# Optimization experiments

Hardware: AMD Instinct MI355X
Metric: run time of the kernel (lower is better)

The kernel has to match this reference:

```python
import jax, jax.numpy as jnp
import numpy as np

D_MODEL = 256
D_HEAD = 64
N_HEAD = 8


def setup_inputs() -> dict:
    key = jax.random.key(0)
    ks = jax.random.split(key, 8)
    b, h, w = 32, 64, 64
    dk = D_HEAD * N_HEAD
    s = 1.0 / np.sqrt(D_MODEL)
    x = jax.random.normal(ks[0], (b, D_MODEL, h, w), dtype=jnp.float32)
    query = jax.random.normal(ks[1], (b, D_MODEL), dtype=jnp.float32)
    Wkv = jax.random.uniform(ks[2], (2 * dk, D_MODEL), jnp.float32, -s, s)
    bkv = jax.random.uniform(ks[3], (2 * dk,), jnp.float32, -s, s)
    Wq = jax.random.uniform(ks[4], (dk, D_MODEL), jnp.float32, -s, s)
    bq = jax.random.uniform(ks[5], (dk,), jnp.float32, -s, s)
    sf = 1.0 / np.sqrt(dk)
    Wfc = jax.random.uniform(ks[6], (D_MODEL, dk), jnp.float32, -sf, sf)
    bfc = jax.random.uniform(ks[7], (D_MODEL,), jnp.float32, -sf, sf)
    return {"x": x, "query": query, "Wkv": Wkv, "bkv": bkv, "Wq": Wq, "bq": bq, "Wfc": Wfc, "bfc": bfc}


def reference(x, query, Wkv, bkv, Wq, bq, Wfc, bfc):
    b, c, h, w = x.shape
    t = h * w
    scale = 1.0 / np.sqrt(D_HEAD).astype(np.float32)
    # 1x1 conv == per-pixel linear: (b, 2*n*d, t)
    kv = jnp.einsum('bchw,oc->bohw', x, Wkv).reshape(b, 2 * N_HEAD, D_HEAD, t)
    kv = kv + bkv.reshape(1, 2 * N_HEAD, D_HEAD, 1)
    k, v = kv[:, :N_HEAD], kv[:, N_HEAD:]  # each (b, n, d, t)
    q = (query @ Wq.T + bq).reshape(b, N_HEAD, D_HEAD)
    logits = jnp.einsum('bnd,bndj->bnj', q, k) * scale
    attn = jax.nn.softmax(logits, axis=2)
    out = jnp.einsum('bnj,bndj->bnd', attn, v).reshape(b, N_HEAD * D_HEAD)
    return jax.nn.relu(out @ Wfc.T + bfc)
```

## Files before the change

kernel.cpp:

```cpp
#include <hip/hip_runtime.h>
#include <hip/hip_bf16.h>

#define B_     32
#define C_     256
#define T_     4096
#define NH_    8
#define DH_    64

__global__ __launch_bounds__(256) void k_prep(
    const float* __restrict__ query, const float* __restrict__ Wkv,
    const float* __restrict__ bkv, const float* __restrict__ Wq,
    const float* __restrict__ bq, float* __restrict__ qWt,
    float* __restrict__ qb) {
  const int n = blockIdx.x;
  const int b = blockIdx.y;
  const int t = threadIdx.x;
  __shared__ float qrow_s[C_];
  __shared__ float psum[4 * 64];
  __shared__ float qsh[64];
  __shared__ float pb_s[64];

  qrow_s[t] = query[(size_t)b * C_ + t];
  __syncthreads();

  {
    const int d = t & 63, ch = t >> 6;
    const float* wrow = Wq + (size_t)(n * DH_ + d) * C_ + ch * 64;
    const float* qr = qrow_s + ch * 64;
    float s = 0.f;
    #pragma unroll
    for (int c = 0; c < 64; c += 4) {
      float4 w = *(const float4*)(wrow + c);
      s += w.x * qr[c] + w.y * qr[c + 1] + w.z * qr[c + 2] + w.w * qr[c + 3];
    }
    psum[ch * 64 + d] = s;
  }
  __syncthreads();
  if (t < 64)
    qsh[t] = bq[n * DH_ + t] + psum[t] + psum[64 + t] + psum[128 + t] + psum[192 + t];
  __syncthreads();

  const float scale = 0.125f;
  {
    const float* wk = Wkv + (size_t)(n * DH_) * C_ + t;
    float acc = 0.f;
    #pragma unroll 8
    for (int dd = 0; dd < DH_; ++dd) acc += qsh[dd] * wk[(size_t)dd * C_];
    qWt[((size_t)b * C_ + t) * NH_ + n] = acc * scale;
  }
  if (t < 64) pb_s[t] = qsh[t] * bkv[n * DH_ + t];
  __syncthreads();
  if (t == 0) {
    float s = 0.f;
    #pragma unroll 8
    for (int dd = 0; dd < 64; ++dd) s += pb_s[dd];
    qb[b * NH_ + n] = s * scale;
  }
}

__global__ __launch_bounds__(256) void k_logits(
    const float* __restrict__ x, const float* __restrict__ qWt,
    const float* __restrict__ qbv, float* __restrict__ lgpart) {
  const int half = blockIdx.y;
  const int b = blockIdx.z;
  const int t = threadIdx.x;
  const int j = blockIdx.x * 512 + t * 2;
  __shared__ float qws[128 * NH_];

  {
    const float4 v = *(const float4*)(qWt + (size_t)b * (C_ * NH_) + half * 1024 + t * 4);
    *(float4*)(qws + t * 4) = v;
  }
  __syncthreads();

  const float* xb = x + (size_t)b * C_ * T_ + (size_t)(half * 128) * T_ + j;
  const float* qb = qbv + b * NH_;

  float acc0[NH_], acc1[NH_];
  #pragma unroll
  for (int n = 0; n < NH_; ++n) {
    const float init = half ? 0.f : qb[n];
    acc0[n] = init; acc1[n] = init;
  }

  for (int c0 = 0; c0 < 128; c0 += 8) {
    float2 xv[8];
    #pragma unroll
    for (int cc = 0; cc < 8; ++cc)
      xv[cc] = *(const float2*)(xb + (size_t)(c0 + cc) * T_);
    #pragma unroll
    for (int cc = 0; cc < 8; ++cc) {
      const float4 w0 = *(const float4*)(qws + (c0 + cc) * 8);
      const float4 w1 = *(const float4*)(qws + (c0 + cc) * 8 + 4);
      acc0[0] += w0.x * xv[cc].x; acc1[0] += w0.x * xv[cc].y;
      acc0[1] += w0.y * xv[cc].x; acc1[1] += w0.y * xv[cc].y;
      acc0[2] += w0.z * xv[cc].x; acc1[2] += w0.z * xv[cc].y;
      acc0[3] += w0.w * xv[cc].x; acc1[3] += w0.w * xv[cc].y;
      acc0[4] += w1.x * xv[cc].x; acc1[4] += w1.x * xv[cc].y;
      acc0[5] += w1.y * xv[cc].x; acc1[5] += w1.y * xv[cc].y;
      acc0[6] += w1.z * xv[cc].x; acc1[6] += w1.z * xv[cc].y;
      acc0[7] += w1.w * xv[cc].x; acc1[7] += w1.w * xv[cc].y;
    }
  }

  float* lg = lgpart + (((size_t)half * B_ + b) * NH_) * T_ + j;
  #pragma unroll
  for (int n = 0; n < NH_; ++n) {
    float2 o; o.x = acc0[n]; o.y = acc1[n];
    *(float2*)(lg + (size_t)n * T_) = o;
  }
}

__global__ __launch_bounds__(256) void k_softmax(
    const float* __restrict__ lgpart, float* __restrict__ attn) {
  const size_t row = blockIdx.x;
  const float* p0 = lgpart + row * T_;
  const float* p1 = lgpart + ((size_t)B_ * NH_ + row) * T_;
  float* pa = attn + row * T_;
  const int t = threadIdx.x;
  float4 v[4];
  #pragma unroll
  for (int i = 0; i < 4; ++i) {
    float4 a = *(const float4*)(p0 + t * 4 + i * 1024);
    float4 c = *(const float4*)(p1 + t * 4 + i * 1024);
    v[i].x = a.x + c.x; v[i].y = a.y + c.y; v[i].z = a.z + c.z; v[i].w = a.w + c.w;
  }

  float m = -3.4e38f;
  #pragma unroll
  for (int i = 0; i < 4; ++i)
    m = fmaxf(m, fmaxf(fmaxf(v[i].x, v[i].y), fmaxf(v[i].z, v[i].w)));
  #pragma unroll
  for (int o = 32; o >= 1; o >>= 1) m = fmaxf(m, __shfl_xor(m, o));
  __shared__ float sm[4];
  if ((t & 63) == 0) sm[t >> 6] = m;
  __syncthreads();
  m = fmaxf(fmaxf(sm[0], sm[1]), fmaxf(sm[2], sm[3]));

  float s = 0.f;
  #pragma unroll
  for (int i = 0; i < 4; ++i) {
    v[i].x = expf(v[i].x - m); v[i].y = expf(v[i].y - m);
    v[i].z = expf(v[i].z - m); v[i].w = expf(v[i].w - m);
    s += v[i].x + v[i].y + v[i].z + v[i].w;
  }
  #pragma unroll
  for (int o = 32; o >= 1; o >>= 1) s += __shfl_xor(s, o);
  __shared__ float ss[4];
  if ((t & 63) == 0) ss[t >> 6] = s;
  __syncthreads();
  s = ss[0] + ss[1] + ss[2] + ss[3];
  const float inv = 1.0f / s;

  #pragma unroll
  for (int i = 0; i < 4; ++i) {
    v[i].x *= inv; v[i].y *= inv; v[i].z *= inv; v[i].w *= inv;
    *(float4*)(pa + t * 4 + i * 1024) = v[i];
  }
}

#define BJ_  256
#define BJS_ 32
#define XPITCH_ 33
__global__ __launch_bounds__(256) void k_xattn(
    const float* __restrict__ x, const float* __restrict__ attn,
    float* __restrict__ part) {
  const int jt = blockIdx.x;
  const int b  = blockIdx.y;
  const int j0 = jt * BJ_;
  const int t  = threadIdx.x;
  __shared__ float xs[C_ * XPITCH_];

  const float* xb = x + (size_t)b * C_ * T_;
  const float* ab = attn + (size_t)b * NH_ * T_ + j0;

  float acc[NH_];
  #pragma unroll
  for (int n = 0; n < NH_; ++n) acc[n] = 0.f;

  const int cr = t >> 3;
  const int jc = (t & 7) * 4;

  for (int sIt = 0; sIt < BJ_ / BJS_; ++sIt) {
    const int js = sIt * BJS_;
    __syncthreads();
    #pragma unroll
    for (int p = 0; p < 8; ++p) {
      const int c = cr + p * 32;
      float4 vv = *(const float4*)(xb + (size_t)c * T_ + j0 + js + jc);
      float* dst = &xs[c * XPITCH_ + jc];
      dst[0] = vv.x; dst[1] = vv.y; dst[2] = vv.z; dst[3] = vv.w;
    }
    __syncthreads();
    const float* xr = &xs[t * XPITCH_];
    #pragma unroll 4
    for (int jj = 0; jj < BJS_; ++jj) {
      const float xv = xr[jj];
      const int j = js + jj;
      #pragma unroll
      for (int n = 0; n < NH_; ++n)
        acc[n] += ab[(size_t)n * T_ + j] * xv;
    }
  }

  float* pb = part + ((size_t)b * 16 + jt) * (NH_ * C_);
  #pragma unroll
  for (int n = 0; n < NH_; ++n) pb[n * C_ + t] = acc[n];
}

__global__ __launch_bounds__(256) void k_outv(
    const float* __restrict__ part, const float* __restrict__ Wkv,
    const float* __restrict__ bkv, float* __restrict__ outvG) {
  __shared__ float xa_s[4 * C_];
  const int hb = blockIdx.x;
  const int b  = blockIdx.y;
  const int t  = threadIdx.x;

  const float* pb = part + (size_t)b * 16 * (NH_ * C_) + hb * (4 * C_);
  #pragma unroll
  for (int r = 0; r < 4; ++r) {
    const int idx = r * 256 + t;
    float s = 0.f;
    #pragma unroll
    for (int jt = 0; jt < 16; ++jt) s += pb[(size_t)jt * (NH_ * C_) + idx];
    xa_s[idx] = s;
  }
  __syncthreads();

  const int o = hb * 256 + t;
  const float* wrow = Wkv + (size_t)(512 + o) * C_;
  const float* xa = &xa_s[(t >> 6) * C_];
  float s = bkv[512 + o];
  #pragma unroll 8
  for (int c = 0; c < C_; c += 4) {
    float4 w = *(const float4*)(wrow + c);
    s += w.x * xa[c] + w.y * xa[c + 1] + w.z * xa[c + 2] + w.w * xa[c + 3];
  }
  outvG[(size_t)b * 512 + o] = s;
}

__global__ __launch_bounds__(256) void k_fc(
    const float* __restrict__ outvG, const float* __restrict__ Wfc,
    const float* __restrict__ bfc, float* __restrict__ out) {
  __shared__ float ov[512];
  const int b = blockIdx.x;
  const int t = threadIdx.x;
  ov[t] = outvG[(size_t)b * 512 + t];
  ov[256 + t] = outvG[(size_t)b * 512 + 256 + t];
  __syncthreads();

  const float* wrow = Wfc + (size_t)t * 512;
  float s = bfc[t];
  #pragma unroll 8
  for (int o = 0; o < 512; o += 4) {
    float4 w = *(const float4*)(wrow + o);
    s += w.x * ov[o] + w.y * ov[o + 1] + w.z * ov[o + 2] + w.w * ov[o + 3];
  }
  out[(size_t)b * 256 + t] = fmaxf(s, 0.f);
}

extern "C" void kernel_launch(void* const* d_in, const int* in_sizes, int n_in,
                              void* d_out, int out_size, void* d_ws, size_t ws_size,
                              hipStream_t stream) {
  const float* x     = (const float*)d_in[0];
  const float* query = (const float*)d_in[1];
  const float* Wkv   = (const float*)d_in[2];
  const float* bkv   = (const float*)d_in[3];
  const float* Wq    = (const float*)d_in[4];
  const float* bq    = (const float*)d_in[5];
  const float* Wfc   = (const float*)d_in[6];
  const float* bfc   = (const float*)d_in[7];
  float* out = (float*)d_out;
  float* ws  = (float*)d_ws;

  float* qWt    = ws;
  float* qb     = ws + 65536;
  float* lgpart = ws + 66048;
  float* attn   = ws + 2163200;
  float* part   = ws + 3211776;
  float* outvG  = ws + 4260352;

  k_prep   <<<dim3(NH_, B_),   256, 0, stream>>>(query, Wkv, bkv, Wq, bq, qWt, qb);
  k_logits <<<dim3(8, 2, B_),  256, 0, stream>>>(x, qWt, qb, lgpart);
  k_softmax<<<B_ * NH_,        256, 0, stream>>>(lgpart, attn);
  k_xattn  <<<dim3(16, B_),    256, 0, stream>>>(x, attn, part);
  k_outv   <<<dim3(2, B_),     256, 0, stream>>>(part, Wkv, bkv, outvG);
  k_fc     <<<B_,              256, 0, stream>>>(outvG, Wfc, bfc, out);
}
```

Measured before the change: 274.3 us.

## Widen logits per-thread work, double-buffer xattn tiles, split fc rows across threads

Three kernels change at once. k_logits now has each thread handle 4 pixels with float4 loads over 128 threads, halving the block size. k_xattn double-buffers its x tile in shared memory so the next tile's global loads overlap compute, and it reads attn as float4. k_fc splits each output row over two threads joined with a shuffle and doubles the grid to raise parallelism. The costs are more registers in k_logits and twice the shared memory in k_xattn, which may reduce occupancy.

```diff
diff --git a/kernel.cpp b/kernel.cpp
--- a/kernel.cpp
+++ b/kernel.cpp
@@ -58,57 +58,56 @@
   }
 }
 
-__global__ __launch_bounds__(256) void k_logits(
+__global__ __launch_bounds__(128) void k_logits(
     const float* __restrict__ x, const float* __restrict__ qWt,
     const float* __restrict__ qbv, float* __restrict__ lgpart) {
   const int half = blockIdx.y;
   const int b = blockIdx.z;
   const int t = threadIdx.x;
-  const int j = blockIdx.x * 512 + t * 2;
+  const int j = blockIdx.x * 512 + t * 4;
   __shared__ float qws[128 * NH_];
 
   {
-    const float4 v = *(const float4*)(qWt + (size_t)b * (C_ * NH_) + half * 1024 + t * 4);
-    *(float4*)(qws + t * 4) = v;
-  }
-  __syncthreads();
-
-  const float* xb = x + (size_t)b * C_ * T_ + (size_t)(half * 128) * T_ + j;
+    const float* src = qWt + (size_t)b * (C_ * NH_) + half * 1024;
+    *(float4*)(qws + t * 8)     = *(const float4*)(src + t * 8);
+    *(float4*)(qws + t * 8 + 4) = *(const float4*)(src + t * 8 + 4);
+  }
+  __syncthreads();
+
+  const float* xb = x + ((size_t)b * C_ + half * 128) * T_ + j;
   const float* qb = qbv + b * NH_;
 
-  float acc0[NH_], acc1[NH_];
+  float4 acc[NH_];
   #pragma unroll
   for (int n = 0; n < NH_; ++n) {
     const float init = half ? 0.f : qb[n];
-    acc0[n] = init; acc1[n] = init;
-  }
-
+    acc[n].x = init; acc[n].y = init; acc[n].z = init; acc[n].w = init;
+  }
+
+#define FMA8_(W, A) { A.x += (W) * xv4.x; A.y += (W) * xv4.y; \
+                      A.z += (W) * xv4.z; A.w += (W) * xv4.w; }
   for (int c0 = 0; c0 < 128; c0 += 8) {
-    float2 xv[8];
+    float4 xv[8];
     #pragma unroll
     for (int cc = 0; cc < 8; ++cc)
-      xv[cc] = *(const float2*)(xb + (size_t)(c0 + cc) * T_);
+      xv[cc] = *(const float4*)(xb + (size_t)(c0 + cc) * T_);
     #pragma unroll
     for (int cc = 0; cc < 8; ++cc) {
       const float4 w0 = *(const float4*)(qws + (c0 + cc) * 8);
       const float4 w1 = *(const float4*)(qws + (c0 + cc) * 8 + 4);
-      acc0[0] += w0.x * xv[cc].x; acc1[0] += w0.x * xv[cc].y;
-      acc0[1] += w0.y * xv[cc].x; acc1[1] += w0.y * xv[cc].y;
-      acc0[2] += w0.z * xv[cc].x; acc1[2] += w0.z * xv[cc].y;
-      acc0[3] += w0.w * xv[cc].x; acc1[3] += w0.w * xv[cc].y;
-      acc0[4] += w1.x * xv[cc].x; acc1[4] += w1.x * xv[cc].y;
-      acc0[5] += w1.y * xv[cc].x; acc1[5] += w1.y * xv[cc].y;
-      acc0[6] += w1.z * xv[cc].x; acc1[6] += w1.z * xv[cc].y;
-      acc0[7] += w1.w * xv[cc].x; acc1[7] += w1.w * xv[cc].y;
-    }
-  }
+      const float4 xv4 = xv[cc];
+      FMA8_(w0.x, acc[0]); FMA8_(w0.y, acc[1]);
+      FMA8_(w0.z, acc[2]); FMA8_(w0.w, acc[3]);
+      FMA8_(w1.x, acc[4]); FMA8_(w1.y, acc[5]);
+      FMA8_(w1.z, acc[6]); FMA8_(w1.w, acc[7]);
+    }
+  }
+#undef FMA8_
 
   float* lg = lgpart + (((size_t)half * B_ + b) * NH_) * T_ + j;
   #pragma unroll
-  for (int n = 0; n < NH_; ++n) {
-    float2 o; o.x = acc0[n]; o.y = acc1[n];
-    *(float2*)(lg + (size_t)n * T_) = o;
-  }
+  for (int n = 0; n < NH_; ++n)
+    *(float4*)(lg + (size_t)n * T_) = acc[n];
 }
 
 __global__ __launch_bounds__(256) void k_softmax(
@@ -169,7 +168,7 @@
   const int b  = blockIdx.y;
   const int j0 = jt * BJ_;
   const int t  = threadIdx.x;
-  __shared__ float xs[C_ * XPITCH_];
+  __shared__ float xs[2][C_ * XPITCH_];
 
   const float* xb = x + (size_t)b * C_ * T_;
   const float* ab = attn + (size_t)b * NH_ * T_ + j0;
@@ -181,26 +180,51 @@
   const int cr = t >> 3;
   const int jc = (t & 7) * 4;
 
+  {
+    float4 v[8];
+    #pragma unroll
+    for (int p = 0; p < 8; ++p)
+      v[p] = *(const float4*)(xb + (size_t)(cr + p * 32) * T_ + j0 + jc);
+    #pragma unroll
+    for (int p = 0; p < 8; ++p) {
+      float* dst = &xs[0][(cr + p * 32) * XPITCH_ + jc];
+      dst[0] = v[p].x; dst[1] = v[p].y; dst[2] = v[p].z; dst[3] = v[p].w;
+    }
+  }
+  __syncthreads();
+
   for (int sIt = 0; sIt < BJ_ / BJS_; ++sIt) {
-    const int js = sIt * BJS_;
+    const int buf = sIt & 1;
+    float4 v[8];
+    if (sIt < BJ_ / BJS_ - 1) {
+      const int js = (sIt + 1) * BJS_;
+      #pragma unroll
+      for (int p = 0; p < 8; ++p)
+        v[p] = *(const float4*)(xb + (size_t)(cr + p * 32) * T_ + j0 + js + jc);
+    }
+
+    const float* xr = &xs[buf][t * XPITCH_];
+    const int jsc = sIt * BJS_;
+    #pragma unroll
+    for (int jg = 0; jg < BJS_ / 4; ++jg) {
+      const int j4 = jg * 4;
+      const float x0 = xr[j4 + 0], x1 = xr[j4 + 1];
+      const float x2 = xr[j4 + 2], x3 = xr[j4 + 3];
+      #pragma unroll
+      for (int n = 0; n < NH_; ++n) {
+        const float4 a = *(const float4*)(ab + (size_t)n * T_ + jsc + j4);
+        acc[n] += a.x * x0 + a.y * x1 + a.z * x2 + a.w * x3;
+      }
+    }
+
+    if (sIt < BJ_ / BJS_ - 1) {
+      #pragma unroll
+      for (int p = 0; p < 8; ++p) {
+        float* dst = &xs[buf ^ 1][(cr + p * 32) * XPITCH_ + jc];
+        dst[0] = v[p].x; dst[1] = v[p].y; dst[2] = v[p].z; dst[3] = v[p].w;
+      }
+    }
     __syncthreads();
-    #pragma unroll
-    for (int p = 0; p < 8; ++p) {
-      const int c = cr + p * 32;
-      float4 vv = *(const float4*)(xb + (size_t)c * T_ + j0 + js + jc);
-      float* dst = &xs[c * XPITCH_ + jc];
-      dst[0] = vv.x; dst[1] = vv.y; dst[2] = vv.z; dst[3] = vv.w;
-    }
-    __syncthreads();
-    const float* xr = &xs[t * XPITCH_];
-    #pragma unroll 4
-    for (int jj = 0; jj < BJS_; ++jj) {
-      const float xv = xr[jj];
-      const int j = js + jj;
-      #pragma unroll
-      for (int n = 0; n < NH_; ++n)
-        acc[n] += ab[(size_t)n * T_ + j] * xv;
-    }
   }
 
   float* pb = part + ((size_t)b * 16 + jt) * (NH_ * C_);
@@ -243,20 +267,25 @@
     const float* __restrict__ outvG, const float* __restrict__ Wfc,
     const float* __restrict__ bfc, float* __restrict__ out) {
   __shared__ float ov[512];
-  const int b = blockIdx.x;
-  const int t = threadIdx.x;
+  const int hx = blockIdx.x;
+  const int b  = blockIdx.y;
+  const int t  = threadIdx.x;
   ov[t] = outvG[(size_t)b * 512 + t];
   ov[256 + t] = outvG[(size_t)b * 512 + 256 + t];
   __syncthreads();
 
-  const float* wrow = Wfc + (size_t)t * 512;
-  float s = bfc[t];
+  const int m    = hx * 128 + (t >> 1);
+  const int half = t & 1;
+  const float* wrow = Wfc + (size_t)m * 512 + half * 256;
+  const float* o = ov + half * 256;
+  float s = half ? 0.f : bfc[m];
   #pragma unroll 8
-  for (int o = 0; o < 512; o += 4) {
-    float4 w = *(const float4*)(wrow + o);
-    s += w.x * ov[o] + w.y * ov[o + 1] + w.z * ov[o + 2] + w.w * ov[o + 3];
-  }
-  out[(size_t)b * 256 + t] = fmaxf(s, 0.f);
+  for (int c = 0; c < 256; c += 4) {
+    float4 w = *(const float4*)(wrow + c);
+    s += w.x * o[c] + w.y * o[c + 1] + w.z * o[c + 2] + w.w * o[c + 3];
+  }
+  s += __shfl_xor(s, 1);
+  if (!half) out[(size_t)b * 256 + m] = fmaxf(s, 0.f);
 }
 
 extern "C" void kernel_launch(void* const* d_in, const int* in_sizes, int n_in,
@@ -281,9 +310,9 @@
   float* outvG  = ws + 4260352;
 
   k_prep   <<<dim3(NH_, B_),   256, 0, stream>>>(query, Wkv, bkv, Wq, bq, qWt, qb);
-  k_logits <<<dim3(8, 2, B_),  256, 0, stream>>>(x, qWt, qb, lgpart);
+  k_logits <<<dim3(8, 2, B_),  128, 0, stream>>>(x, qWt, qb, lgpart);
   k_softmax<<<B_ * NH_,        256, 0, stream>>>(lgpart, attn);
   k_xattn  <<<dim3(16, B_),    256, 0, stream>>>(x, attn, part);
   k_outv   <<<dim3(2, B_),     256, 0, stream>>>(part, Wkv, bkv, outvG);
-  k_fc     <<<B_,              256, 0, stream>>>(outvG, Wfc, bfc, out);
-}
+  k_fc     <<<dim3(2, B_),     256, 0, stream>>>(outvG, Wfc, bfc, out);
+}
```

New measurement: 279.0 us. No clear change (+1.7%).
